# Kernel optimization log

Measured on AMD Instinct MI355X. Metric: run time of the kernel, lower is better.

Reference implementation:

```python
import jax, jax.numpy as jnp
import numpy as np

HIDDEN = 3584
H = 28          # num attention heads
KV = 4          # num key-value heads
HD = 128        # head dim
MROPE = [16, 24, 24]  # sum*2 == HD
EPS = 1e-6
S_TOT = 4096
N_SAMPLES = 4


def rmsnorm(x, w, eps=EPS):
    return x * jax.lax.rsqrt(jnp.mean(x * x, axis=-1, keepdims=True) + eps) * w


def rotate_half(x):
    x1, x2 = jnp.split(x, 2, axis=-1)
    return jnp.concatenate([-x2, x1], axis=-1)


def mrope_merge(t):
    # t: [3, S, HD] -> [S, HD], section i taken from rope axis i%3
    cuts = np.cumsum(np.array(MROPE) * 2)[:-1]
    parts = jnp.split(t, cuts, axis=-1)
    return jnp.concatenate([p[i % 3] for i, p in enumerate(parts)], axis=-1)


def setup_inputs() -> dict:
    key = jax.random.key(0)
    ks = iter(jax.random.split(key, 32))
    std = 0.02

    def w(shape):
        return jax.random.normal(next(ks), shape, dtype=jnp.float32) * std

    inp = {
        "packed_sequence": jax.random.normal(next(ks), (S_TOT, HIDDEN), dtype=jnp.float32),
        "packed_cos": jax.random.uniform(next(ks), (3, S_TOT, HD), dtype=jnp.float32, minval=-1.0, maxval=1.0),
        "packed_sin": jax.random.uniform(next(ks), (3, S_TOT, HD), dtype=jnp.float32, minval=-1.0, maxval=1.0),
    }
    # und / geo indices partition [0, S_TOT)
    inp["packed_und_token_indexes"] = jnp.arange(S_TOT // 2, dtype=jnp.int64 if jax.config.jax_enable_x64 else jnp.int32)
    inp["packed_geo_token_indexes"] = jnp.arange(S_TOT // 2, dtype=inp["packed_und_token_indexes"].dtype) + S_TOT // 2
    inp["sample_len"] = S_TOT // N_SAMPLES

    for tag in ("und", "geo"):
        inp[f"q_w_{tag}"] = w((H * HD, HIDDEN))
        inp[f"q_b_{tag}"] = jnp.zeros((H * HD,), jnp.float32)
        inp[f"k_w_{tag}"] = w((KV * HD, HIDDEN))
        inp[f"k_b_{tag}"] = jnp.zeros((KV * HD,), jnp.float32)
        inp[f"v_w_{tag}"] = w((KV * HD, HIDDEN))
        inp[f"v_b_{tag}"] = jnp.zeros((KV * HD,), jnp.float32)
        inp[f"o_w_{tag}"] = w((HIDDEN, H * HD))
        inp[f"q_norm_{tag}"] = jnp.ones((HD,), jnp.float32)
        inp[f"k_norm_{tag}"] = jnp.ones((HD,), jnp.float32)
    return inp


def reference(packed_sequence, packed_cos, packed_sin,
              q_w_und, q_b_und, k_w_und, k_b_und, v_w_und, v_b_und, o_w_und,
              q_norm_und, k_norm_und,
              q_w_geo, q_b_geo, k_w_geo, k_b_geo, v_w_geo, v_b_geo, o_w_geo,
              q_norm_geo, k_norm_geo,
              packed_und_token_indexes, packed_geo_token_indexes, sample_len):
    S, D = packed_sequence.shape
    G = H // KV
    und, geo = packed_und_token_indexes, packed_geo_token_indexes
    xu = packed_sequence[und]
    xg = packed_sequence[geo]

    def scatter(dim, fu, fg):
        out = jnp.zeros((S, dim), packed_sequence.dtype)
        return out.at[und].set(fu).at[geo].set(fg)

    # modality-routed QKV projections (gather -> gemm -> scatter)
    q = scatter(H * HD, xu @ q_w_und.T + q_b_und, xg @ q_w_geo.T + q_b_geo).reshape(S, H, HD)
    k = scatter(KV * HD, xu @ k_w_und.T + k_b_und, xg @ k_w_geo.T + k_b_geo).reshape(S, KV, HD)
    v = scatter(KV * HD, xu @ v_w_und.T + v_b_und, xg @ v_w_geo.T + v_b_geo).reshape(S, KV, HD)

    # per-modality QK RMSNorm
    qn = jnp.zeros_like(q).at[und].set(rmsnorm(q[und], q_norm_und)).at[geo].set(rmsnorm(q[geo], q_norm_geo))
    kn = jnp.zeros_like(k).at[und].set(rmsnorm(k[und], k_norm_und)).at[geo].set(rmsnorm(k[geo], k_norm_geo))

    # multimodal rotary embedding
    cos = mrope_merge(packed_cos)[:, None, :]  # [S,1,HD]
    sin = mrope_merge(packed_sin)[:, None, :]
    qr = qn * cos + rotate_half(qn) * sin
    kr = kn * cos + rotate_half(kn) * sin

    # block-diagonal causal attention over packed equal-length samples
    L = int(sample_len)
    B = S // L
    qb = qr.reshape(B, L, H, HD)
    kb = jnp.repeat(kr.reshape(B, L, KV, HD), G, axis=2)  # GQA expansion
    vb = jnp.repeat(v.reshape(B, L, KV, HD), G, axis=2)
    scores = jnp.einsum('blhd,bmhd->bhlm', qb, kb) / np.sqrt(HD).astype(np.float32)
    causal = jnp.tril(jnp.ones((L, L), bool))
    scores = jnp.where(causal, scores, jnp.finfo(scores.dtype).min)
    attn = jax.nn.softmax(scores, axis=-1)
    out = jnp.einsum('bhlm,bmhd->blhd', attn, vb).reshape(S, H * HD)

    # modality-routed output projection
    res = jnp.zeros((S, D), packed_sequence.dtype)
    res = res.at[und].set(out[und] @ o_w_und.T).at[geo].set(out[geo] @ o_w_geo.T)
    return res
```

## Files before the change

### kernel.cpp

```cpp
#include <hip/hip_runtime.h>
#include <hip/hip_bf16.h>
#include <stdint.h>

#define HIDDEN 3584
#define NH 28
#define NKV 4
#define HD 128
#define GQ (NH / NKV)
#define NQKV ((NH + 2 * NKV) * HD)
#define LSAMP 1024

typedef __bf16 bf16x8 __attribute__((ext_vector_type(8)));
typedef float f32x4 __attribute__((ext_vector_type(4)));

__device__ __forceinline__ unsigned short f2bf(float f) {
  unsigned int u = __float_as_uint(f);
  u += 0x7fffu + ((u >> 16) & 1u);
  return (unsigned short)(u >> 16);
}
__device__ __forceinline__ float bf2f(unsigned short h) {
  return __uint_as_float(((unsigned int)h) << 16);
}

__device__ __forceinline__ void gload16(const void* g, void* l) {
  __builtin_amdgcn_global_load_lds(
      (const __attribute__((address_space(1))) void*)g,
      (__attribute__((address_space(3))) void*)l, 16, 0, 0);
}

__global__ void build_maps_kernel(const int* __restrict__ und, const int* __restrict__ geo,
                                  int nu, int ng,
                                  int* __restrict__ row_of_token, int* __restrict__ tok_of_row,
                                  int* __restrict__ mod_of_token) {
  int i = blockIdx.x * 256 + threadIdx.x;
  if (i < nu) {
    int t = und[i];
    row_of_token[t] = i; tok_of_row[i] = t; mod_of_token[t] = 0;
  } else if (i < nu + ng) {
    int j = i - nu;
    int t = geo[j];
    row_of_token[t] = nu + j; tok_of_row[nu + j] = t; mod_of_token[t] = 1;
  }
}

struct Cvt8 {
  const float* src[8];
  unsigned short* dst[8];
  int cum[8];
};
__global__ void convert8_kernel(Cvt8 a, int tot4) {
  int i = blockIdx.x * blockDim.x + threadIdx.x;
  const int stride = gridDim.x * blockDim.x;
  for (; i < tot4; i += stride) {
    int seg = 0;
#pragma unroll
    for (int s2 = 1; s2 < 8; ++s2) seg += (i >= a.cum[s2]);
    const int off = i - a.cum[seg];
    float4 v = reinterpret_cast<const float4*>(a.src[seg])[off];
    reinterpret_cast<ushort4*>(a.dst[seg])[off] =
        make_ushort4(f2bf(v.x), f2bf(v.y), f2bf(v.z), f2bf(v.w));
  }
}

__global__ void gather_x_kernel(const float* __restrict__ X, const int* __restrict__ tok_of_row,
                                unsigned short* __restrict__ Xg) {
  const int r = blockIdx.x;
  const int tok = tok_of_row[r];
  const float4* src = reinterpret_cast<const float4*>(X + (size_t)tok * HIDDEN);
  ushort4* dst = reinterpret_cast<ushort4*>(Xg + (size_t)r * HIDDEN);
  for (int i = threadIdx.x; i < HIDDEN / 4; i += 256) {
    float4 v = src[i];
    dst[i] = make_ushort4(f2bf(v.x), f2bf(v.y), f2bf(v.z), f2bf(v.w));
  }
}

template <int OUTMODE, int NT, int WR, int WC, int NF>
__global__ __launch_bounds__(NT, (NT / 64 + 3) / 4)
void gemm2_kernel(const unsigned short* __restrict__ A,
                  const unsigned short* __restrict__ W0, const unsigned short* __restrict__ W1,
                  const float* __restrict__ qb0, const float* __restrict__ kb0, const float* __restrict__ vb0,
                  const float* __restrict__ qb1, const float* __restrict__ kb1, const float* __restrict__ vb1,
                  unsigned short* __restrict__ Obf, float* __restrict__ Of32,
                  const int* __restrict__ tok_of_row,
                  int nu, int ng, int N, int K, int NX, int NY) {
  constexpr int MF = 256 / WR / 16;
  constexpr int BN = WC * NF * 16;
  constexpr int BUFSZ = 32768 + BN * 128;
  constexpr int ACH = 2048;
  constexpr int BCH = BN * 8;
  __shared__ char lds[2 * BUFSZ];

  const int nwg = NX * NY * 2;
  int id = blockIdx.x + NX * (blockIdx.y + NY * blockIdx.z);
  {
    const int q = nwg >> 3, r = nwg & 7;
    const int xcd = id & 7, pos = id >> 3;
    id = (xcd < r ? xcd * (q + 1) : r * (q + 1) + (xcd - r) * q) + pos;
  }
  const int bx = id % NX;
  const int byz = id / NX;
  const int by = byz % NY;
  const int bz = byz / NY;

  const int baseRow = bz ? nu : 0;
  const int Mcount = bz ? ng : nu;
  const int mbase = by * 256;
  if (mbase >= Mcount) return;
  const unsigned short* W = bz ? W1 : W0;

  const int t = threadIdx.x;
  const int w = t >> 6, l = t & 63;
  const int l15 = l & 15, l4 = l >> 4;
  const int wr = w / WC, wc = w % WC;
  const int wrr = wr * (MF * 16), wcc = wc * (NF * 16);
  const int ncol0 = bx * BN;

  f32x4 acc[MF][NF] = {};

  const int nk = K >> 6;

  auto stage = [&](int bufIdx, int kt) {
    char* base = lds + bufIdx * BUFSZ;
    const int k0 = kt * 64;
#pragma unroll
    for (int c0 = 0; c0 < ACH; c0 += NT) {
      const int c = c0 + t;
      if (c < ACH) {
        const int row = c >> 3, slot = c & 7;
        const int srck = (slot ^ (row & 7)) << 3;
        int ar = mbase + row; if (ar >= Mcount) ar = Mcount - 1;
        gload16(A + (size_t)(baseRow + ar) * K + k0 + srck, base + c * 16);
      }
    }
#pragma unroll
    for (int c0 = 0; c0 < BCH; c0 += NT) {
      const int c = c0 + t;
      if (c < BCH) {
        const int row = c >> 3, slot = c & 7;
        const int srck = (slot ^ (row & 7)) << 3;
        gload16(W + (size_t)(ncol0 + row) * K + k0 + srck, base + 32768 + c * 16);
      }
    }
  };

  stage(0, 0);
  asm volatile("s_waitcnt vmcnt(0)\n\ts_barrier" ::: "memory");

  for (int kt = 0; kt < nk; ++kt) {
    char* Ab = lds + (kt & 1) * BUFSZ;
    char* Bb = Ab + 32768;

    if (kt + 1 < nk) stage((kt + 1) & 1, kt + 1);
    __builtin_amdgcn_sched_barrier(0);

#pragma unroll
    for (int ks = 0; ks < 2; ++ks) {
      bf16x8 af[MF], bfr[NF];
#pragma unroll
      for (int mf = 0; mf < MF; ++mf) {
        const int row = wrr + mf * 16 + l15;
        af[mf] = *reinterpret_cast<const bf16x8*>(Ab + row * 128 + (((ks * 4 + l4) ^ (row & 7)) << 4));
      }
#pragma unroll
      for (int nf = 0; nf < NF; ++nf) {
        const int row = wcc + nf * 16 + l15;
        bfr[nf] = *reinterpret_cast<const bf16x8*>(Bb + row * 128 + (((ks * 4 + l4) ^ (row & 7)) << 4));
      }
      __builtin_amdgcn_s_setprio(1);
#pragma unroll
      for (int mf = 0; mf < MF; ++mf)
#pragma unroll
        for (int nf = 0; nf < NF; ++nf)
          acc[mf][nf] = __builtin_amdgcn_mfma_f32_16x16x32_bf16(af[mf], bfr[nf], acc[mf][nf], 0, 0, 0);
      __builtin_amdgcn_s_setprio(0);
    }

    if (kt + 1 < nk) {
      asm volatile("s_waitcnt vmcnt(0)\n\ts_barrier" ::: "memory");
    }
  }

#pragma unroll
  for (int mf = 0; mf < MF; ++mf) {
#pragma unroll
    for (int rr = 0; rr < 4; ++rr) {
      const int ml = mbase + wrr + mf * 16 + l4 * 4 + rr;
      if (ml >= Mcount) continue;
      int trow = 0;
      if (OUTMODE == 1) trow = tok_of_row[baseRow + ml];
#pragma unroll
      for (int nf = 0; nf < NF; ++nf) {
        const int n = ncol0 + wcc + nf * 16 + l15;
        const float v = acc[mf][nf][rr];
        if (OUTMODE == 0) {
          const float* qb = bz ? qb1 : qb0;
          const float* kb = bz ? kb1 : kb0;
          const float* vb = bz ? vb1 : vb0;
          const float bias = (n < NH * HD) ? qb[n]
                              : ((n < (NH + NKV) * HD) ? kb[n - NH * HD] : vb[n - (NH + NKV) * HD]);
          Obf[(size_t)(baseRow + ml) * N + n] = f2bf(v + bias);
        } else {
          Of32[(size_t)trow * N + n] = v;
        }
      }
    }
  }
}

__global__ __launch_bounds__(64)
void norm_rope_kernel(const unsigned short* __restrict__ Y,
                      const int* __restrict__ row_of_token, const int* __restrict__ mod_of_token,
                      const float* __restrict__ pcos, const float* __restrict__ psin,
                      const float* __restrict__ qn_u, const float* __restrict__ kn_u,
                      const float* __restrict__ qn_g, const float* __restrict__ kn_g,
                      unsigned short* __restrict__ Qr,
                      unsigned short* __restrict__ Kr,
                      unsigned short* __restrict__ Vt,
                      int S) {
  const int s = blockIdx.x, t = threadIdx.x;
  const int r = row_of_token[s];
  const int m = mod_of_token[s];
  const float* qn = m ? qn_g : qn_u;
  const float* kn = m ? kn_g : kn_u;
  const int d0 = t, d1 = t + 64;
  const int a0 = (d0 < 32) ? 0 : (d0 < 80 ? 1 : 2);
  const int a1 = (d1 < 80) ? 1 : 2;
  const float c0 = pcos[((size_t)a0 * S + s) * HD + d0];
  const float c1 = pcos[((size_t)a1 * S + s) * HD + d1];
  const float s0 = psin[((size_t)a0 * S + s) * HD + d0];
  const float s1 = psin[((size_t)a1 * S + s) * HD + d1];
  const float qnw0 = qn[t], qnw1 = qn[t + 64];
  const float knw0 = kn[t], knw1 = kn[t + 64];
  const unsigned short* yrow = Y + (size_t)r * NQKV;
  constexpr float SC = 0.08838834764831845f;

#pragma unroll 4
  for (int hh = 0; hh < NH; ++hh) {
    float x0 = bf2f(yrow[hh * HD + t]);
    float x1 = bf2f(yrow[hh * HD + t + 64]);
    float ss = x0 * x0 + x1 * x1;
#pragma unroll
    for (int dd = 1; dd < 64; dd <<= 1) ss += __shfl_xor(ss, dd);
    const float rs = rsqrtf(ss * (1.f / 128.f) + 1e-6f);
    const float q0 = x0 * rs * qnw0, q1 = x1 * rs * qnw1;
    unsigned short* dst = Qr + ((size_t)hh * S + s) * HD;
    dst[t] = f2bf((q0 * c0 - q1 * s0) * SC);
    dst[t + 64] = f2bf((q1 * c1 + q0 * s1) * SC);
  }
#pragma unroll
  for (int kh = 0; kh < NKV; ++kh) {
    float x0 = bf2f(yrow[NH * HD + kh * HD + t]);
    float x1 = bf2f(yrow[NH * HD + kh * HD + t + 64]);
    float ss = x0 * x0 + x1 * x1;
#pragma unroll
    for (int dd = 1; dd < 64; dd <<= 1) ss += __shfl_xor(ss, dd);
    const float rs = rsqrtf(ss * (1.f / 128.f) + 1e-6f);
    const float k0 = x0 * rs * knw0, k1 = x1 * rs * knw1;
    unsigned short* dst = Kr + ((size_t)kh * S + s) * HD;
    dst[t] = f2bf(k0 * c0 - k1 * s0);
    dst[t + 64] = f2bf(k1 * c1 + k0 * s1);
  }
#pragma unroll
  for (int vh = 0; vh < NKV; ++vh) {
    float x0 = bf2f(yrow[(NH + NKV) * HD + vh * HD + t]);
    float x1 = bf2f(yrow[(NH + NKV) * HD + vh * HD + t + 64]);
    Vt[((size_t)(vh * HD + t)) * S + s] = f2bf(x0);
    Vt[((size_t)(vh * HD + t + 64)) * S + s] = f2bf(x1);
  }
}

__global__ __launch_bounds__(256, 2)
void attn_kernel(const unsigned short* __restrict__ Qr, const unsigned short* __restrict__ Kr,
                 const unsigned short* __restrict__ Vt, const int* __restrict__ row_of_token,
                 unsigned short* __restrict__ Og, int S, int NXQ) {
  __shared__ char lds[2 * 16384 + 2 * 16384 + 64 * 144];
  char* Plds = lds + 65536;
  const int h = blockIdx.y, b = blockIdx.z;
  const int kvh = h / GQ;
  const int t = threadIdx.x, w = t >> 6, l = t & 63;
  const int l15 = l & 15, l4 = l >> 4;
  const int sbase = b * LSAMP;

  auto stage = [&](int bufIdx, int kt) {
    char* Kb = lds + bufIdx * 16384;
    char* Vb = lds + 32768 + bufIdx * 16384;
    const int kb0 = sbase + kt * 64;
#pragma unroll
    for (int i = 0; i < 4; ++i) {
      const int c = t + i * 256;
      const int row = c >> 4, slot = c & 15;
      const int srcs = slot ^ (row & 15);
      gload16(Kr + ((size_t)kvh * S + kb0 + row) * HD + srcs * 8, Kb + c * 16);
    }
#pragma unroll
    for (int i = 0; i < 4; ++i) {
      const int c = t + i * 256;
      const int row = c >> 3, slot = c & 7;
      const int srcs = slot ^ (row & 7);
      gload16(Vt + (size_t)(kvh * HD + row) * S + kb0 + srcs * 8, Vb + c * 16);
    }
  };

  for (int pass = 0; pass < 2; ++pass) {
    const int qt = pass ? (NXQ - 1 - blockIdx.x) : blockIdx.x;

    bf16x8 aq[4];
    {
      const int qrow = sbase + qt * 64 + w * 16 + l15;
      const unsigned short* qp = Qr + ((size_t)h * S + qrow) * HD + l4 * 8;
#pragma unroll
      for (int kk = 0; kk < 4; ++kk) aq[kk] = *reinterpret_cast<const bf16x8*>(qp + kk * 32);
    }
    f32x4 acc[8] = {};
    float mr[4] = {-INFINITY, -INFINITY, -INFINITY, -INFINITY};
    float lr[4] = {0.f, 0.f, 0.f, 0.f};

    stage(0, 0);
    asm volatile("s_waitcnt vmcnt(0)\n\ts_barrier" ::: "memory");

    for (int kt = 0; kt <= qt; ++kt) {
      char* Kb = lds + (kt & 1) * 16384;
      char* Vb = lds + 32768 + (kt & 1) * 16384;

      if (kt < qt) stage((kt + 1) & 1, kt + 1);
      __builtin_amdgcn_sched_barrier(0);

      f32x4 sa[4] = {};
#pragma unroll
      for (int kk = 0; kk < 4; ++kk) {
        bf16x8 bk[4];
#pragma unroll
        for (int nf = 0; nf < 4; ++nf) {
          const int row = nf * 16 + l15;
          const int slot = kk * 4 + l4;
          bk[nf] = *reinterpret_cast<const bf16x8*>(Kb + row * 256 + ((slot ^ (row & 15)) << 4));
        }
#pragma unroll
        for (int nf = 0; nf < 4; ++nf)
          sa[nf] = __builtin_amdgcn_mfma_f32_16x16x32_bf16(aq[kk], bk[nf], sa[nf], 0, 0, 0);
      }

      const int qg = qt * 64 + w * 16 + l4 * 4;
#pragma unroll
      for (int nf = 0; nf < 4; ++nf) {
        const int cg = kt * 64 + nf * 16 + l15;
#pragma unroll
        for (int rr = 0; rr < 4; ++rr)
          if (cg > qg + rr) sa[nf][rr] = -INFINITY;
      }

      float pv[4][4];
#pragma unroll
      for (int rr = 0; rr < 4; ++rr) {
        float mx = fmaxf(fmaxf(sa[0][rr], sa[1][rr]), fmaxf(sa[2][rr], sa[3][rr]));
        mx = fmaxf(mx, mr[rr]);
#pragma unroll
        for (int dd = 1; dd < 16; dd <<= 1) mx = fmaxf(mx, __shfl_xor(mx, dd));
        const float alpha = __expf(mr[rr] - mx);
        mr[rr] = mx;
        float part = 0.f;
#pragma unroll
        for (int nf = 0; nf < 4; ++nf) {
          const float p = __expf(sa[nf][rr] - mx);
          pv[nf][rr] = p;
          part += p;
        }
        lr[rr] = lr[rr] * alpha + part;
#pragma unroll
        for (int nf2 = 0; nf2 < 8; ++nf2) acc[nf2][rr] *= alpha;
      }

#pragma unroll
      for (int rr = 0; rr < 4; ++rr) {
        const int row = w * 16 + l4 * 4 + rr;
#pragma unroll
        for (int nf = 0; nf < 4; ++nf)
          ((unsigned short*)(Plds + row * 144))[nf * 16 + l15] = f2bf(pv[nf][rr]);
      }

#pragma unroll
      for (int kk2 = 0; kk2 < 2; ++kk2) {
        const bf16x8 ap = *reinterpret_cast<const bf16x8*>(Plds + (w * 16 + l15) * 144 + kk2 * 64 + l4 * 16);
#pragma unroll
        for (int nf2 = 0; nf2 < 8; ++nf2) {
          const int rowd = nf2 * 16 + l15;
          const int slot = kk2 * 4 + l4;
          const bf16x8 bv = *reinterpret_cast<const bf16x8*>(Vb + rowd * 128 + ((slot ^ (rowd & 7)) << 4));
          acc[nf2] = __builtin_amdgcn_mfma_f32_16x16x32_bf16(ap, bv, acc[nf2], 0, 0, 0);
        }
      }

      if (kt < qt) {
        asm volatile("s_waitcnt vmcnt(0)\n\ts_barrier" ::: "memory");
      }
    }

#pragma unroll
    for (int rr = 0; rr < 4; ++rr)
#pragma unroll
      for (int dd = 1; dd < 16; dd <<= 1) lr[rr] += __shfl_xor(lr[rr], dd);

    const int srow0 = sbase + qt * 64 + w * 16 + l4 * 4;
#pragma unroll
    for (int rr = 0; rr < 4; ++rr) {
      const float inv = 1.f / lr[rr];
      const int mrow = row_of_token[srow0 + rr];
      unsigned short* orow = Og + (size_t)mrow * (NH * HD) + h * HD;
#pragma unroll
      for (int nf2 = 0; nf2 < 8; ++nf2) orow[nf2 * 16 + l15] = f2bf(acc[nf2][rr] * inv);
    }

    if (pass == 0) {
      asm volatile("s_waitcnt vmcnt(0) lgkmcnt(0)\n\ts_barrier" ::: "memory");
    }
  }
}

extern "C" void kernel_launch(void* const* d_in, const int* in_sizes, int n_in,
                              void* d_out, int out_size, void* d_ws, size_t ws_size,
                              hipStream_t stream) {
  const float* X = (const float*)d_in[0];
  const float* pcos = (const float*)d_in[1];
  const float* psin = (const float*)d_in[2];
  const int* und = (const int*)d_in[3];
  const int* geo = (const int*)d_in[4];
  const int nu = in_sizes[3], ng = in_sizes[4];
  const int S = in_sizes[0] / HIDDEN;

  const float* qw[2] = {(const float*)d_in[6], (const float*)d_in[15]};
  const float* qb[2] = {(const float*)d_in[7], (const float*)d_in[16]};
  const float* kw[2] = {(const float*)d_in[8], (const float*)d_in[17]};
  const float* kb[2] = {(const float*)d_in[9], (const float*)d_in[18]};
  const float* vw[2] = {(const float*)d_in[10], (const float*)d_in[19]};
  const float* vb[2] = {(const float*)d_in[11], (const float*)d_in[20]};
  const float* ow[2] = {(const float*)d_in[12], (const float*)d_in[21]};
  const float* qn[2] = {(const float*)d_in[13], (const float*)d_in[22]};
  const float* kn[2] = {(const float*)d_in[14], (const float*)d_in[23]};

  char* ws = (char*)d_ws;
  size_t off = 0;
  auto alloc = [&](size_t bytes) {
    char* p = ws + off;
    off = (off + bytes + 255) & ~(size_t)255;
    return p;
  };
  int* row_of_token = (int*)alloc((size_t)S * 4);
  int* tok_of_row = (int*)alloc((size_t)S * 4);
  int* mod_of_token = (int*)alloc((size_t)S * 4);
  unsigned short* Wqkv[2] = {(unsigned short*)alloc((size_t)NQKV * HIDDEN * 2),
                             (unsigned short*)alloc((size_t)NQKV * HIDDEN * 2)};
  unsigned short* Wo[2] = {(unsigned short*)alloc((size_t)HIDDEN * HIDDEN * 2),
                           (unsigned short*)alloc((size_t)HIDDEN * HIDDEN * 2)};
  unsigned short* Xg = (unsigned short*)alloc((size_t)S * HIDDEN * 2);
  unsigned short* Yqkv = (unsigned short*)alloc((size_t)S * NQKV * 2);
  unsigned short* Qr = (unsigned short*)alloc((size_t)NH * S * HD * 2);
  unsigned short* Kr = (unsigned short*)alloc((size_t)NKV * S * HD * 2);
  unsigned short* Vt = (unsigned short*)alloc((size_t)NKV * S * HD * 2);
  unsigned short* Og = (unsigned short*)alloc((size_t)S * NH * HD * 2);
  (void)ws_size; (void)n_in; (void)out_size;

  build_maps_kernel<<<(S + 255) / 256, 256, 0, stream>>>(und, geo, nu, ng,
                                                         row_of_token, tok_of_row, mod_of_token);
  {
    Cvt8 ca;
    const float* srcs[8] = {qw[0], kw[0], vw[0], ow[0], qw[1], kw[1], vw[1], ow[1]};
    unsigned short* dsts[8] = {
        Wqkv[0], Wqkv[0] + (size_t)NH * HD * HIDDEN, Wqkv[0] + (size_t)(NH + NKV) * HD * HIDDEN, Wo[0],
        Wqkv[1], Wqkv[1] + (size_t)NH * HD * HIDDEN, Wqkv[1] + (size_t)(NH + NKV) * HD * HIDDEN, Wo[1]};
    const int n4s[8] = {NH * HD * HIDDEN / 4, NKV * HD * HIDDEN / 4, NKV * HD * HIDDEN / 4, HIDDEN * HIDDEN / 4,
                        NH * HD * HIDDEN / 4, NKV * HD * HIDDEN / 4, NKV * HD * HIDDEN / 4, HIDDEN * HIDDEN / 4};
    int cum = 0;
    for (int i = 0; i < 8; ++i) { ca.src[i] = srcs[i]; ca.dst[i] = dsts[i]; ca.cum[i] = cum; cum += n4s[i]; }
    convert8_kernel<<<2048, 256, 0, stream>>>(ca, cum);
  }
  gather_x_kernel<<<S, 256, 0, stream>>>(X, tok_of_row, Xg);

  const int maxM = (nu > ng ? nu : ng);
  {
    const int NX = NQKV / 288, NY = (maxM + 255) / 256;
    gemm2_kernel<0, 768, 4, 3, 6><<<dim3(NX, NY, 2), 768, 0, stream>>>(
        Xg, Wqkv[0], Wqkv[1], qb[0], kb[0], vb[0], qb[1], kb[1], vb[1],
        Yqkv, nullptr, nullptr, nu, ng, NQKV, HIDDEN, NX, NY);
  }

  norm_rope_kernel<<<S, 64, 0, stream>>>(Yqkv, row_of_token, mod_of_token, pcos, psin,
                                         qn[0], kn[0], qn[1], kn[1], Qr, Kr, Vt, S);

  {
    const int NXQ = LSAMP / 64;
    attn_kernel<<<dim3(NXQ / 2, NH, S / LSAMP), 256, 0, stream>>>(Qr, Kr, Vt, row_of_token, Og, S, NXQ);
  }

  {
    const int NX = HIDDEN / 224, NY = (maxM + 255) / 256;
    gemm2_kernel<1, 512, 4, 2, 7><<<dim3(NX, NY, 2), 512, 0, stream>>>(
        Og, Wo[0], Wo[1], nullptr, nullptr, nullptr, nullptr, nullptr, nullptr,
        nullptr, (float*)d_out, tok_of_row, nu, ng, HIDDEN, HIDDEN, NX, NY);
  }
}
```

Measured before the change: 409.1 us.

## Split A/B staging in GEMM mainloop and prefetch A two tiles ahead

The GEMM mainloop now stages the A tile two iterations ahead and the B tile one iteration ahead, and waits with partial vmcnt counts instead of draining all outstanding loads. The MFMA work is split into sub-blocks over B fragments so LDS reads interleave with matrix ops, and a mid-iteration barrier lets the next A prefetch reuse the current buffer. This is meant to hide global-load latency and shorten barrier stalls in both the QKV and output projections. The cost is more complex synchronisation, with hardcoded vmcnt literals tied to the per-thread load count, and redundant wrapped loads when the chunk count does not divide evenly by the thread count.

```diff
diff --git a/kernel.cpp b/kernel.cpp
--- a/kernel.cpp
+++ b/kernel.cpp
@@ -74,9 +74,9 @@
   }
 }
 
-template <int OUTMODE, int NT, int WR, int WC, int NF>
+template <int OUTMODE, int NT, int WR, int WC, int NF, int NFA>
 __global__ __launch_bounds__(NT, (NT / 64 + 3) / 4)
-void gemm2_kernel(const unsigned short* __restrict__ A,
+void gemm8_kernel(const unsigned short* __restrict__ A,
                   const unsigned short* __restrict__ W0, const unsigned short* __restrict__ W1,
                   const float* __restrict__ qb0, const float* __restrict__ kb0, const float* __restrict__ vb0,
                   const float* __restrict__ qb1, const float* __restrict__ kb1, const float* __restrict__ vb1,
@@ -85,9 +85,14 @@
                   int nu, int ng, int N, int K, int NX, int NY) {
   constexpr int MF = 256 / WR / 16;
   constexpr int BN = WC * NF * 16;
-  constexpr int BUFSZ = 32768 + BN * 128;
+  constexpr int ABYTES = 32768;
+  constexpr int BBYTES = BN * 128;
+  constexpr int BUFSZ = ABYTES + BBYTES;
   constexpr int ACH = 2048;
   constexpr int BCH = BN * 8;
+  constexpr int LA = (ACH + NT - 1) / NT;
+  constexpr int LB = (BCH + NT - 1) / NT;
+  static_assert(LA == 3 || LA == 4, "vmcnt literal specialization");
   __shared__ char lds[2 * BUFSZ];
 
   const int nwg = NX * NY * 2;
@@ -116,67 +121,121 @@
   const int ncol0 = bx * BN;
 
   f32x4 acc[MF][NF] = {};
-
   const int nk = K >> 6;
 
-  auto stage = [&](int bufIdx, int kt) {
+  auto stageA = [&](int bufIdx, int kt) {
     char* base = lds + bufIdx * BUFSZ;
     const int k0 = kt * 64;
 #pragma unroll
-    for (int c0 = 0; c0 < ACH; c0 += NT) {
-      const int c = c0 + t;
-      if (c < ACH) {
-        const int row = c >> 3, slot = c & 7;
-        const int srck = (slot ^ (row & 7)) << 3;
-        int ar = mbase + row; if (ar >= Mcount) ar = Mcount - 1;
-        gload16(A + (size_t)(baseRow + ar) * K + k0 + srck, base + c * 16);
-      }
-    }
-#pragma unroll
-    for (int c0 = 0; c0 < BCH; c0 += NT) {
-      const int c = c0 + t;
-      if (c < BCH) {
-        const int row = c >> 3, slot = c & 7;
-        const int srck = (slot ^ (row & 7)) << 3;
-        gload16(W + (size_t)(ncol0 + row) * K + k0 + srck, base + 32768 + c * 16);
-      }
+    for (int i = 0; i < LA; ++i) {
+      int c = t + i * NT; if (c >= ACH) c -= ACH;
+      const int row = c >> 3, slot = c & 7;
+      const int srck = (slot ^ (row & 7)) << 3;
+      int ar = mbase + row; if (ar >= Mcount) ar = Mcount - 1;
+      gload16(A + (size_t)(baseRow + ar) * K + k0 + srck, base + c * 16);
     }
   };
-
-  stage(0, 0);
-  asm volatile("s_waitcnt vmcnt(0)\n\ts_barrier" ::: "memory");
+  auto stageB = [&](int bufIdx, int kt) {
+    char* base = lds + bufIdx * BUFSZ + ABYTES;
+    const int k0 = kt * 64;
+#pragma unroll
+    for (int i = 0; i < LB; ++i) {
+      int c = t + i * NT; if (c >= BCH) c -= BCH;
+      const int row = c >> 3, slot = c & 7;
+      const int srck = (slot ^ (row & 7)) << 3;
+      gload16(W + (size_t)(ncol0 + row) * K + k0 + srck, base + c * 16);
+    }
+  };
+
+  stageA(0, 0); stageB(0, 0); stageA(1, 1);
+  if (nk > 1) {
+    if constexpr (LA == 3) asm volatile("s_waitcnt vmcnt(3)\n\ts_barrier" ::: "memory");
+    else                   asm volatile("s_waitcnt vmcnt(4)\n\ts_barrier" ::: "memory");
+  } else {
+    asm volatile("s_waitcnt vmcnt(0)\n\ts_barrier" ::: "memory");
+  }
 
   for (int kt = 0; kt < nk; ++kt) {
-    char* Ab = lds + (kt & 1) * BUFSZ;
-    char* Bb = Ab + 32768;
-
-    if (kt + 1 < nk) stage((kt + 1) & 1, kt + 1);
+    const int cur = kt & 1;
+    char* Ab = lds + cur * BUFSZ;
+    char* Bb = Ab + ABYTES;
+    bf16x8 af[MF], b0[NFA], b1[NF - NFA];
+
+    if (kt + 1 < nk) stageB(cur ^ 1, kt + 1);
     __builtin_amdgcn_sched_barrier(0);
-
-#pragma unroll
-    for (int ks = 0; ks < 2; ++ks) {
-      bf16x8 af[MF], bfr[NF];
-#pragma unroll
-      for (int mf = 0; mf < MF; ++mf) {
-        const int row = wrr + mf * 16 + l15;
-        af[mf] = *reinterpret_cast<const bf16x8*>(Ab + row * 128 + (((ks * 4 + l4) ^ (row & 7)) << 4));
-      }
-#pragma unroll
-      for (int nf = 0; nf < NF; ++nf) {
-        const int row = wcc + nf * 16 + l15;
-        bfr[nf] = *reinterpret_cast<const bf16x8*>(Bb + row * 128 + (((ks * 4 + l4) ^ (row & 7)) << 4));
-      }
-      __builtin_amdgcn_s_setprio(1);
-#pragma unroll
-      for (int mf = 0; mf < MF; ++mf)
-#pragma unroll
-        for (int nf = 0; nf < NF; ++nf)
-          acc[mf][nf] = __builtin_amdgcn_mfma_f32_16x16x32_bf16(af[mf], bfr[nf], acc[mf][nf], 0, 0, 0);
-      __builtin_amdgcn_s_setprio(0);
-    }
+#pragma unroll
+    for (int mf = 0; mf < MF; ++mf) {
+      const int row = wrr + mf * 16 + l15;
+      af[mf] = *reinterpret_cast<const bf16x8*>(Ab + row * 128 + (((l4) ^ (row & 7)) << 4));
+    }
+#pragma unroll
+    for (int j = 0; j < NFA; ++j) {
+      const int row = wcc + j * 16 + l15;
+      b0[j] = *reinterpret_cast<const bf16x8*>(Bb + row * 128 + (((l4) ^ (row & 7)) << 4));
+    }
+    __builtin_amdgcn_s_setprio(1);
+#pragma unroll
+    for (int mf = 0; mf < MF; ++mf)
+#pragma unroll
+      for (int j = 0; j < NFA; ++j)
+        acc[mf][j] = __builtin_amdgcn_mfma_f32_16x16x32_bf16(af[mf], b0[j], acc[mf][j], 0, 0, 0);
+    __builtin_amdgcn_s_setprio(0);
+
+#pragma unroll
+    for (int j = 0; j < NF - NFA; ++j) {
+      const int row = wcc + (NFA + j) * 16 + l15;
+      b1[j] = *reinterpret_cast<const bf16x8*>(Bb + row * 128 + (((l4) ^ (row & 7)) << 4));
+    }
+    __builtin_amdgcn_s_setprio(1);
+#pragma unroll
+    for (int mf = 0; mf < MF; ++mf)
+#pragma unroll
+      for (int j = 0; j < NF - NFA; ++j)
+        acc[mf][NFA + j] = __builtin_amdgcn_mfma_f32_16x16x32_bf16(af[mf], b1[j], acc[mf][NFA + j], 0, 0, 0);
+    __builtin_amdgcn_s_setprio(0);
+
+#pragma unroll
+    for (int mf = 0; mf < MF; ++mf) {
+      const int row = wrr + mf * 16 + l15;
+      af[mf] = *reinterpret_cast<const bf16x8*>(Ab + row * 128 + (((4 + l4) ^ (row & 7)) << 4));
+    }
+#pragma unroll
+    for (int j = 0; j < NFA; ++j) {
+      const int row = wcc + j * 16 + l15;
+      b0[j] = *reinterpret_cast<const bf16x8*>(Bb + row * 128 + (((4 + l4) ^ (row & 7)) << 4));
+    }
+    __builtin_amdgcn_s_setprio(1);
+#pragma unroll
+    for (int mf = 0; mf < MF; ++mf)
+#pragma unroll
+      for (int j = 0; j < NFA; ++j)
+        acc[mf][j] = __builtin_amdgcn_mfma_f32_16x16x32_bf16(af[mf], b0[j], acc[mf][j], 0, 0, 0);
+    __builtin_amdgcn_s_setprio(0);
+
+    asm volatile("s_barrier" ::: "memory");
+
+    if (kt + 2 < nk) stageA(cur, kt + 2);
+    __builtin_amdgcn_sched_barrier(0);
+#pragma unroll
+    for (int j = 0; j < NF - NFA; ++j) {
+      const int row = wcc + (NFA + j) * 16 + l15;
+      b1[j] = *reinterpret_cast<const bf16x8*>(Bb + row * 128 + (((4 + l4) ^ (row & 7)) << 4));
+    }
+    __builtin_amdgcn_s_setprio(1);
+#pragma unroll
+    for (int mf = 0; mf < MF; ++mf)
+#pragma unroll
+      for (int j = 0; j < NF - NFA; ++j)
+        acc[mf][NFA + j] = __builtin_amdgcn_mfma_f32_16x16x32_bf16(af[mf], b1[j], acc[mf][NFA + j], 0, 0, 0);
+    __builtin_amdgcn_s_setprio(0);
 
     if (kt + 1 < nk) {
-      asm volatile("s_waitcnt vmcnt(0)\n\ts_barrier" ::: "memory");
+      if (kt + 2 < nk) {
+        if constexpr (LA == 3) asm volatile("s_waitcnt vmcnt(3)\n\ts_barrier" ::: "memory");
+        else                   asm volatile("s_waitcnt vmcnt(4)\n\ts_barrier" ::: "memory");
+      } else {
+        asm volatile("s_waitcnt vmcnt(0)\n\ts_barrier" ::: "memory");
+      }
     }
   }
 
@@ -478,7 +537,7 @@
   const int maxM = (nu > ng ? nu : ng);
   {
     const int NX = NQKV / 288, NY = (maxM + 255) / 256;
-    gemm2_kernel<0, 768, 4, 3, 6><<<dim3(NX, NY, 2), 768, 0, stream>>>(
+    gemm8_kernel<0, 768, 4, 3, 6, 3><<<dim3(NX, NY, 2), 768, 0, stream>>>(
         Xg, Wqkv[0], Wqkv[1], qb[0], kb[0], vb[0], qb[1], kb[1], vb[1],
         Yqkv, nullptr, nullptr, nu, ng, NQKV, HIDDEN, NX, NY);
   }
@@ -493,7 +552,7 @@
 
   {
     const int NX = HIDDEN / 224, NY = (maxM + 255) / 256;
-    gemm2_kernel<1, 512, 4, 2, 7><<<dim3(NX, NY, 2), 512, 0, stream>>>(
+    gemm8_kernel<1, 512, 4, 2, 7, 4><<<dim3(NX, NY, 2), 512, 0, stream>>>(
         Og, Wo[0], Wo[1], nullptr, nullptr, nullptr, nullptr, nullptr, nullptr,
         nullptr, (float*)d_out, tok_of_row, nu, ng, HIDDEN, HIDDEN, NX, NY);
   }
```

Result: no change. 410.0 us (+0.2%).

## Load GEMM A operand directly into registers, staging only weights in LDS

Applied to the files above, without the earlier changes.

The shared GEMM kernel no longer stages the activation (A) tile through LDS. Each wave now reads its own A fragments from global memory into registers, and only the weight (B) tile stays double-buffered in LDS. The aim is to cut LDS traffic and footprint and drop the A-side LDS reads. In exchange, waves in the same row group fetch the same A rows redundantly. The next tile's A loads are issued only after the current compute, so their global latency may be poorly hidden. The hardcoded vmcnt(8) depends on exactly eight A loads being in flight.

```diff
diff --git a/kernel.cpp b/kernel.cpp
--- a/kernel.cpp
+++ b/kernel.cpp
@@ -76,7 +76,7 @@
 
 template <int OUTMODE, int NT, int WR, int WC, int NF>
 __global__ __launch_bounds__(NT, (NT / 64 + 3) / 4)
-void gemm2_kernel(const unsigned short* __restrict__ A,
+void gemmA_kernel(const unsigned short* __restrict__ A,
                   const unsigned short* __restrict__ W0, const unsigned short* __restrict__ W1,
                   const float* __restrict__ qb0, const float* __restrict__ kb0, const float* __restrict__ vb0,
                   const float* __restrict__ qb1, const float* __restrict__ kb1, const float* __restrict__ vb1,
@@ -85,10 +85,11 @@
                   int nu, int ng, int N, int K, int NX, int NY) {
   constexpr int MF = 256 / WR / 16;
   constexpr int BN = WC * NF * 16;
-  constexpr int BUFSZ = 32768 + BN * 128;
-  constexpr int ACH = 2048;
+  constexpr int BBYTES = BN * 128;
   constexpr int BCH = BN * 8;
-  __shared__ char lds[2 * BUFSZ];
+  constexpr int LB = (BCH + NT - 1) / NT;
+  static_assert(MF * 2 == 8, "vmcnt literal below assumes 8 A-loads in flight");
+  __shared__ char lds[2 * BBYTES];
 
   const int nwg = NX * NY * 2;
   int id = blockIdx.x + NX * (blockIdx.y + NY * blockIdx.z);
@@ -116,51 +117,47 @@
   const int ncol0 = bx * BN;
 
   f32x4 acc[MF][NF] = {};
-
   const int nk = K >> 6;
 
-  auto stage = [&](int bufIdx, int kt) {
-    char* base = lds + bufIdx * BUFSZ;
+  const unsigned short* aptr[MF];
+#pragma unroll
+  for (int mf = 0; mf < MF; ++mf) {
+    int ar = mbase + wrr + mf * 16 + l15;
+    if (ar >= Mcount) ar = Mcount - 1;
+    aptr[mf] = A + (size_t)(baseRow + ar) * K + l4 * 8;
+  }
+
+  auto stageB = [&](int bufIdx, int kt) {
+    char* base = lds + bufIdx * BBYTES;
     const int k0 = kt * 64;
 #pragma unroll
-    for (int c0 = 0; c0 < ACH; c0 += NT) {
-      const int c = c0 + t;
-      if (c < ACH) {
-        const int row = c >> 3, slot = c & 7;
-        const int srck = (slot ^ (row & 7)) << 3;
-        int ar = mbase + row; if (ar >= Mcount) ar = Mcount - 1;
-        gload16(A + (size_t)(baseRow + ar) * K + k0 + srck, base + c * 16);
-      }
-    }
-#pragma unroll
-    for (int c0 = 0; c0 < BCH; c0 += NT) {
-      const int c = c0 + t;
-      if (c < BCH) {
-        const int row = c >> 3, slot = c & 7;
-        const int srck = (slot ^ (row & 7)) << 3;
-        gload16(W + (size_t)(ncol0 + row) * K + k0 + srck, base + 32768 + c * 16);
-      }
+    for (int i = 0; i < LB; ++i) {
+      int c = t + i * NT; if (c >= BCH) c -= BCH;
+      const int row = c >> 3, slot = c & 7;
+      const int srck = (slot ^ (row & 7)) << 3;
+      gload16(W + (size_t)(ncol0 + row) * K + k0 + srck, base + c * 16);
     }
   };
 
-  stage(0, 0);
-  asm volatile("s_waitcnt vmcnt(0)\n\ts_barrier" ::: "memory");
+  bf16x8 afC[MF][2];
+
+  stageB(0, 0);
+#pragma unroll
+  for (int mf = 0; mf < MF; ++mf) {
+    afC[mf][0] = *reinterpret_cast<const bf16x8*>(aptr[mf]);
+    afC[mf][1] = *reinterpret_cast<const bf16x8*>(aptr[mf] + 32);
+  }
+  asm volatile("s_waitcnt vmcnt(8)\n\ts_barrier" ::: "memory");
 
   for (int kt = 0; kt < nk; ++kt) {
-    char* Ab = lds + (kt & 1) * BUFSZ;
-    char* Bb = Ab + 32768;
-
-    if (kt + 1 < nk) stage((kt + 1) & 1, kt + 1);
+    char* Bb = lds + (kt & 1) * BBYTES;
+
+    if (kt + 1 < nk) stageB((kt + 1) & 1, kt + 1);
     __builtin_amdgcn_sched_barrier(0);
 
 #pragma unroll
     for (int ks = 0; ks < 2; ++ks) {
-      bf16x8 af[MF], bfr[NF];
-#pragma unroll
-      for (int mf = 0; mf < MF; ++mf) {
-        const int row = wrr + mf * 16 + l15;
-        af[mf] = *reinterpret_cast<const bf16x8*>(Ab + row * 128 + (((ks * 4 + l4) ^ (row & 7)) << 4));
-      }
+      bf16x8 bfr[NF];
 #pragma unroll
       for (int nf = 0; nf < NF; ++nf) {
         const int row = wcc + nf * 16 + l15;
@@ -171,12 +168,18 @@
       for (int mf = 0; mf < MF; ++mf)
 #pragma unroll
         for (int nf = 0; nf < NF; ++nf)
-          acc[mf][nf] = __builtin_amdgcn_mfma_f32_16x16x32_bf16(af[mf], bfr[nf], acc[mf][nf], 0, 0, 0);
+          acc[mf][nf] = __builtin_amdgcn_mfma_f32_16x16x32_bf16(afC[mf][ks], bfr[nf], acc[mf][nf], 0, 0, 0);
       __builtin_amdgcn_s_setprio(0);
     }
 
     if (kt + 1 < nk) {
-      asm volatile("s_waitcnt vmcnt(0)\n\ts_barrier" ::: "memory");
+      const int k0n = (kt + 1) * 64;
+#pragma unroll
+      for (int mf = 0; mf < MF; ++mf) {
+        afC[mf][0] = *reinterpret_cast<const bf16x8*>(aptr[mf] + k0n);
+        afC[mf][1] = *reinterpret_cast<const bf16x8*>(aptr[mf] + k0n + 32);
+      }
+      asm volatile("s_waitcnt vmcnt(8)\n\ts_barrier" ::: "memory");
     }
   }
 
@@ -478,7 +481,7 @@
   const int maxM = (nu > ng ? nu : ng);
   {
     const int NX = NQKV / 288, NY = (maxM + 255) / 256;
-    gemm2_kernel<0, 768, 4, 3, 6><<<dim3(NX, NY, 2), 768, 0, stream>>>(
+    gemmA_kernel<0, 768, 4, 3, 6><<<dim3(NX, NY, 2), 768, 0, stream>>>(
         Xg, Wqkv[0], Wqkv[1], qb[0], kb[0], vb[0], qb[1], kb[1], vb[1],
         Yqkv, nullptr, nullptr, nu, ng, NQKV, HIDDEN, NX, NY);
   }
@@ -493,7 +496,7 @@
 
   {
     const int NX = HIDDEN / 224, NY = (maxM + 255) / 256;
-    gemm2_kernel<1, 512, 4, 2, 7><<<dim3(NX, NY, 2), 512, 0, stream>>>(
+    gemmA_kernel<1, 512, 4, 2, 7><<<dim3(NX, NY, 2), 512, 0, stream>>>(
         Og, Wo[0], Wo[1], nullptr, nullptr, nullptr, nullptr, nullptr, nullptr,
         nullptr, (float*)d_out, tok_of_row, nu, ng, HIDDEN, HIDDEN, NX, NY);
   }
```

Result: slower. 604.5 us (+47.8%).
